# Optimization experiments

Measured on AMD Instinct MI355X. Metric: run time of the kernel, lower is better.

The kernel has to match this reference:

```python
import jax, jax.numpy as jnp
import numpy as np

N_NODES = 30000
N_REL = 8
N_EDGES = 150000
EMB = 128
HID = 128
OUT = 256
HEADS = 4
RANK = 8
SCALE = 1.0
NEG_SLOPE = 0.2
LN_EPS = 1e-5


def setup_inputs():
    key = jax.random.key(0)
    ks = jax.random.split(key, 16)
    def nrm(k, shp, s=0.05):
        return jax.random.normal(k, shp, dtype=jnp.float32) * s
    d2 = HEADS * HID  # conv2 input dim = 512
    return {
        "entity_emb": nrm(ks[0], (N_NODES, EMB)),
        "A1": nrm(ks[1], (N_REL, EMB * RANK)),
        "B1": nrm(ks[2], (N_REL, EMB * RANK)),
        "W1": nrm(ks[3], (HEADS * HID, EMB)),
        "att_l1": nrm(ks[4], (1, HEADS, HID)),
        "att_r1": nrm(ks[5], (1, HEADS, HID)),
        "relb1": jnp.zeros((N_REL, HEADS), jnp.float32),
        "bias1": jnp.zeros((HEADS * HID,), jnp.float32),
        "A2": nrm(ks[6], (N_REL, d2 * RANK)),
        "B2": nrm(ks[7], (N_REL, d2 * RANK)),
        "W2": nrm(ks[8], (OUT, d2)),
        "att_l2": nrm(ks[9], (1, 1, OUT)),
        "att_r2": nrm(ks[10], (1, 1, OUT)),
        "relb2": jnp.zeros((N_REL, 1), jnp.float32),
        "bias2": jnp.zeros((OUT,), jnp.float32),
        "res_W": nrm(ks[11], (OUT, EMB)),
        "res_b": jnp.zeros((OUT,), jnp.float32),
        "ln_g": jnp.ones((OUT,), jnp.float32),
        "ln_b": jnp.zeros((OUT,), jnp.float32),
        "edge_index": jax.random.randint(ks[12], (2, N_EDGES), 0, N_NODES),
        "edge_type": jax.random.randint(ks[13], (N_EDGES,), 0, N_REL),
    }


def _rel_gat_conv(x, A, B, W, att_l, att_r, relb, bias, j_idx, i_idx, etype, heads, out_dim, concat):
    # x: [N,d]; A,B: [R, d*k]; W: [heads*out_dim, d]
    N, d = x.shape
    R = A.shape[0]
    k = RANK
    HC = heads * out_dim
    A3 = A.reshape(R, d, k)
    B3 = B.reshape(R, d, k)
    z_all = x @ W.T  # [N, HC] base linear (shared by z_i and z_j)
    # LoRA low-rank projection per (node, relation): P[n,r] = B_r^T x_n
    P = jnp.einsum('nd,rdk->nrk', x, B3)          # [N,R,k] (small)
    low = P[j_idx, etype]                          # [E,k]
    # Fused LoRA-through-lin: lin(scale*A_r B_r^T x) = scale * low @ (A_r^T W^T)
    M = jnp.einsum('rdk,hd->rkh', A3, W).reshape(R * k, HC)  # [R*k, HC]
    oh = jax.nn.one_hot(etype, R, dtype=x.dtype)   # [E,R]
    low_exp = (oh[:, :, None] * low[:, None, :]).reshape(-1, R * k)  # [E,R*k]
    z_j = (z_all[j_idx] + SCALE * (low_exp @ M)).reshape(-1, heads, out_dim)  # [E,H,C]
    z_i = z_all[i_idx].reshape(-1, heads, out_dim)                            # [E,H,C]
    alpha = (z_i * att_l).sum(-1) + (z_j * att_r).sum(-1) + relb[etype]       # [E,H]
    alpha = jax.nn.leaky_relu(alpha, NEG_SLOPE)
    # per-relation loop => softmax groups are (relation, target node)
    seg = etype * N + i_idx
    n_seg = R * N
    amax = jax.ops.segment_max(alpha, seg, num_segments=n_seg)
    ex = jnp.exp(alpha - amax[seg])
    den = jax.ops.segment_sum(ex, seg, num_segments=n_seg)
    alpha = ex / den[seg]
    msg = z_j * alpha[:, :, None]                  # [E,H,C]
    out = jax.ops.segment_sum(msg, i_idx, num_segments=N)  # [N,H,C]
    out = out.reshape(N, HC) if concat else out.mean(axis=1)
    return out + bias


def _forward(entity_emb, A1, B1, W1, att_l1, att_r1, relb1, bias1,
             A2, B2, W2, att_l2, att_r2, relb2, bias2,
             res_W, res_b, ln_g, ln_b, edge_index, edge_type):
    j_idx, i_idx = edge_index[0], edge_index[1]
    x0 = entity_emb
    x = _rel_gat_conv(x0, A1, B1, W1, att_l1, att_r1, relb1, bias1,
                      j_idx, i_idx, edge_type, HEADS, HID, True)
    x = jax.nn.elu(x)
    x = _rel_gat_conv(x, A2, B2, W2, att_l2, att_r2, relb2, bias2,
                      j_idx, i_idx, edge_type, 1, OUT, False)
    x = x + (x0 @ res_W.T + res_b)
    mu = x.mean(axis=-1, keepdims=True)
    var = ((x - mu) ** 2).mean(axis=-1, keepdims=True)
    return (x - mu) / jnp.sqrt(var + LN_EPS) * ln_g + ln_b


def reference(entity_emb, A1, B1, W1, att_l1, att_r1, relb1, bias1,
              A2, B2, W2, att_l2, att_r2, relb2, bias2,
              res_W, res_b, ln_g, ln_b, edge_index, edge_type):
    return _forward(entity_emb, A1, B1, W1, att_l1, att_r1, relb1, bias1,
                    A2, B2, W2, att_l2, att_r2, relb2, bias2,
                    res_W, res_b, ln_g, ln_b, edge_index, edge_type)
```

## Files before the change

kernel.cpp:

```cpp
#include <hip/hip_runtime.h>
#include <cstddef>

#define NRELS 8
#define EMB 128
#define HID 128
#define OUTD 256
#define HEADS 4
#define RANK 8
#define D2 512
#define KCAT 192
#define NEG_SLOPE 0.2f
#define LN_EPS 1e-5f
#define JMASK 0x07FFFFFFu

typedef short bf16x8 __attribute__((ext_vector_type(8)));
typedef float f32x4 __attribute__((ext_vector_type(4)));

__device__ __forceinline__ unsigned short f2bf(float f) {
  union { float f; unsigned u; } v; v.f = f;
  unsigned u = v.u;
  return (unsigned short)((u + 0x7fffu + ((u >> 16) & 1u)) >> 16);
}
__device__ __forceinline__ float bf2f(unsigned short u) {
  union { unsigned u; float f; } v; v.u = (unsigned)u << 16; return v.f;
}
__device__ __forceinline__ unsigned pk2(float a, float b) {
  return (unsigned)f2bf(a) | ((unsigned)f2bf(b) << 16);
}
__device__ __forceinline__ unsigned asu(float f) { return __float_as_uint(f); }

#define GLOAD16(ldsp, gp) \
  __builtin_amdgcn_global_load_lds((const __attribute__((address_space(1))) unsigned int*)(gp), \
      (__attribute__((address_space(3))) unsigned int*)(ldsp), 16, 0, 0)

template<int BIAS, int F32OUT, int ELU, int PB>
__device__ __forceinline__ void gemm_tile_body(unsigned short* AsB, unsigned short* BsB,
    int bx, int by, int ny,
    const unsigned short* __restrict__ A, const unsigned short* __restrict__ B,
    unsigned short* __restrict__ C, float* __restrict__ Cf,
    const unsigned short* __restrict__ Bp, float* __restrict__ Cp,
    int M, int N, int K, int lda, int aoffc,
    const float* __restrict__ bias, const float* __restrict__ b1p) {
  const int tid = threadIdx.x;
  const int wave = tid >> 6;
  const int lane = tid & 63;
  const int wm = wave & 1;
  const int wn = wave >> 1;
  const int r16 = lane & 15;
  const int quad = lane >> 4;
  const int bm = bx * 128;
  const int lr = lane >> 2;
  const int lc = ((lane & 3) ^ ((lane >> 3) & 3)) * 8;
  const int rsw = (quad ^ ((r16 >> 1) & 3)) * 8;
  const bool isP = PB && (by == ny - 1);
  const unsigned short* Bu = isP ? Bp : B;
  const int bn = isP ? 0 : by * 128;
  const unsigned short* Abase = A + (size_t)by * (isP ? 0 : aoffc);
  int ar0 = bm + wave * 32 + lr;      if (ar0 >= M) ar0 = M - 1;
  int ar1 = bm + wave * 32 + 16 + lr; if (ar1 >= M) ar1 = M - 1;
  const unsigned short* Ag0 = Abase + (size_t)ar0 * lda + lc;
  const unsigned short* Ag1 = Abase + (size_t)ar1 * lda + lc;
  const unsigned short* Bg0 = Bu + (size_t)(bn + wave * 32 + lr) * K + lc;
  const unsigned short* Bg1 = Bu + (size_t)(bn + wave * 32 + 16 + lr) * K + lc;
  f32x4 acc[4][4] = {};
  GLOAD16(AsB + wave * 1024, Ag0);
  GLOAD16(AsB + wave * 1024 + 512, Ag1);
  GLOAD16(BsB + wave * 1024, Bg0);
  GLOAD16(BsB + wave * 1024 + 512, Bg1);
  __syncthreads();
  int cur = 0;
  for (int k0 = 0; k0 < K; k0 += 32) {
    if (k0 + 32 < K) {
      GLOAD16(AsB + (cur ^ 1) * 4096 + wave * 1024, Ag0 + k0 + 32);
      GLOAD16(AsB + (cur ^ 1) * 4096 + wave * 1024 + 512, Ag1 + k0 + 32);
      GLOAD16(BsB + (cur ^ 1) * 4096 + wave * 1024, Bg0 + k0 + 32);
      GLOAD16(BsB + (cur ^ 1) * 4096 + wave * 1024 + 512, Bg1 + k0 + 32);
    }
    bf16x8 af[4], bfr[4];
#pragma unroll
    for (int mi = 0; mi < 4; ++mi)
      af[mi] = *(const bf16x8*)(AsB + cur * 4096 + (wm * 64 + mi * 16 + r16) * 32 + rsw);
#pragma unroll
    for (int ni = 0; ni < 4; ++ni)
      bfr[ni] = *(const bf16x8*)(BsB + cur * 4096 + (wn * 64 + ni * 16 + r16) * 32 + rsw);
#pragma unroll
    for (int mi = 0; mi < 4; ++mi)
#pragma unroll
      for (int ni = 0; ni < 4; ++ni)
        acc[mi][ni] = __builtin_amdgcn_mfma_f32_16x16x32_bf16(af[mi], bfr[ni], acc[mi][ni], 0, 0, 0);
    __syncthreads();
    cur ^= 1;
  }
  float bcol[4];
  if (BIAS) {
#pragma unroll
    for (int ni = 0; ni < 4; ++ni) {
      int cn = bn + wn * 64 + ni * 16 + r16;
      bcol[ni] = bias[cn];
      if (F32OUT) bcol[ni] += b1p[cn];
    }
  }
#pragma unroll
  for (int mi = 0; mi < 4; ++mi)
#pragma unroll
    for (int ni = 0; ni < 4; ++ni)
#pragma unroll
      for (int r = 0; r < 4; ++r) {
        int row = bm + wm * 64 + mi * 16 + quad * 4 + r;
        if (row < M) {
          int col = wn * 64 + ni * 16 + r16;
          float v = acc[mi][ni][r];
          if (isP) {
            Cp[(size_t)row * 128 + col] = v;
          } else {
            if (BIAS) v += bcol[ni];
            if (ELU) v = v > 0.f ? v : expm1f(v);
            size_t idx = (size_t)row * N + bn + col;
            if (F32OUT) Cf[idx] = v;
            else        C[idx] = f2bf(v);
          }
        }
      }
}

template<int BIAS, int F32OUT, int ELU, int PB>
__global__ __launch_bounds__(256) void gemm_tile(const unsigned short* __restrict__ A,
    const unsigned short* __restrict__ B, unsigned short* __restrict__ C,
    float* __restrict__ Cf, const unsigned short* __restrict__ Bp,
    float* __restrict__ Cp, int M, int N, int K, int lda, int aoffc,
    const float* __restrict__ bias, const float* __restrict__ b1p) {
  __shared__ unsigned short As[2 * 4096];
  __shared__ unsigned short Bs[2 * 4096];
  gemm_tile_body<BIAS, F32OUT, ELU, PB>(As, Bs, blockIdx.x, blockIdx.y, gridDim.y,
      A, B, C, Cf, Bp, Cp, M, N, K, lda, aoffc, bias, b1p);
}

__global__ __launch_bounds__(256) void combo_abt_p1(const float* __restrict__ Amat1,
    const float* __restrict__ W1, float* __restrict__ M1o,
    const float* __restrict__ Amat2, const float* __restrict__ W2, float* __restrict__ M2o,
    const unsigned short* __restrict__ x0b, const unsigned short* __restrict__ Bp1ext,
    float* __restrict__ Cp1, int Nn) {
  __shared__ unsigned short GA[2 * 4096];
  __shared__ unsigned short GB[2 * 4096];
  const int bx = blockIdx.x;
  if (bx < 12) {
    float* As_ = (float*)GA;
    float* Bs_ = (float*)GB;
    const float* A; const float* B; float* C; int N, K, bn;
    if (bx < 8) { A = Amat1; B = W1; C = M1o; N = D2; K = EMB; bn = bx * 64; }
    else { A = Amat2; B = W2; C = M2o; N = OUTD; K = D2; bn = (bx - 8) * 64; }
    const int tid = threadIdx.x;
    const int tx = tid & 15;
    const int ty = tid >> 4;
    const int lr2 = tid & 63;
    const int lq = tid >> 6;
    float acc[4][4] = {};
    for (int k0 = 0; k0 < K; k0 += 32) {
#pragma unroll
      for (int s = 0; s < 2; ++s) {
        const int q = lq + s * 4;
        float4 va = *(const float4*)(A + (size_t)lr2 * K + k0 + q * 4);
        As_[(q * 4 + 0) * 64 + lr2] = va.x; As_[(q * 4 + 1) * 64 + lr2] = va.y;
        As_[(q * 4 + 2) * 64 + lr2] = va.z; As_[(q * 4 + 3) * 64 + lr2] = va.w;
        float4 vb = *(const float4*)(B + (size_t)(bn + lr2) * K + k0 + q * 4);
        Bs_[(q * 4 + 0) * 64 + lr2] = vb.x; Bs_[(q * 4 + 1) * 64 + lr2] = vb.y;
        Bs_[(q * 4 + 2) * 64 + lr2] = vb.z; Bs_[(q * 4 + 3) * 64 + lr2] = vb.w;
      }
      __syncthreads();
#pragma unroll
      for (int kk = 0; kk < 32; ++kk) {
        float a[4], b[4];
#pragma unroll
        for (int i2 = 0; i2 < 4; ++i2) { a[i2] = As_[kk * 64 + ty * 4 + i2]; b[i2] = Bs_[kk * 64 + tx * 4 + i2]; }
#pragma unroll
        for (int i2 = 0; i2 < 4; ++i2)
#pragma unroll
          for (int j2 = 0; j2 < 4; ++j2)
            acc[i2][j2] = fmaf(a[i2], b[j2], acc[i2][j2]);
      }
      __syncthreads();
    }
#pragma unroll
    for (int i2 = 0; i2 < 4; ++i2)
#pragma unroll
      for (int j2 = 0; j2 < 4; ++j2)
        C[(size_t)(ty * 4 + i2) * N + bn + tx * 4 + j2] = acc[i2][j2];
  } else {
    gemm_tile_body<0, 1, 0, 0>(GA, GB, bx - 12, 0, 1, x0b, Bp1ext, nullptr, Cp1,
                               nullptr, nullptr, Nn, 128, EMB, EMB, 0, nullptr, nullptr);
  }
}

__global__ void prep_all(const float* __restrict__ x0, const float* __restrict__ W1,
    const float* __restrict__ W2, const float* __restrict__ res_W,
    const float* __restrict__ A1, const float* __restrict__ A2,
    const float* __restrict__ B1, const float* __restrict__ B2,
    const float* __restrict__ attL1, const float* __restrict__ attR1,
    const float* __restrict__ attL2, const float* __restrict__ attR2,
    unsigned short* __restrict__ x0b, unsigned short* __restrict__ Acat,
    unsigned short* __restrict__ W2b, unsigned short* __restrict__ RWcat,
    float* __restrict__ Amat1, float* __restrict__ Amat2,
    unsigned short* __restrict__ Bp1ext, unsigned short* __restrict__ Bp2ext,
    unsigned short* __restrict__ Bcat1,
    float* __restrict__ awR1f, float* __restrict__ awR2f,
    const int* __restrict__ ii, int* __restrict__ ideg, int* __restrict__ prepos,
    int E, int nx0) {
  int idx = blockIdx.x * 256 + threadIdx.x;
  if (idx < E) { prepos[idx] = atomicAdd(&ideg[ii[idx]], 1); return; } idx -= E;
  if (idx < nx0) { unsigned short b = f2bf(x0[idx]); x0b[idx] = b;
    Acat[(size_t)(idx >> 7) * KCAT + (idx & 127)] = b; return; } idx -= nx0;
  if (idx < OUTD * D2) { W2b[idx] = f2bf(W2[idx]); return; } idx -= OUTD * D2;
  if (idx < OUTD * EMB) { RWcat[(size_t)(idx >> 7) * KCAT + (idx & 127)] = f2bf(res_W[idx]); return; } idx -= OUTD * EMB;
  if (idx < 64 * EMB) { int d = idx % EMB, rk = idx / EMB, k = rk & 7, r = rk >> 3;
    Amat1[idx] = A1[(size_t)r * EMB * RANK + (size_t)d * RANK + k]; return; } idx -= 64 * EMB;
  if (idx < 64 * D2) { int d = idx % D2, rk = idx / D2, k = rk & 7, r = rk >> 3;
    Amat2[idx] = A2[(size_t)r * D2 * RANK + (size_t)d * RANK + k]; return; } idx -= 64 * D2;
  if (idx < 64 * EMB) { int d = idx % EMB, rk = idx / EMB, k = rk & 7, r = rk >> 3;
    Bp1ext[idx] = f2bf(B1[(size_t)r * EMB * RANK + (size_t)d * RANK + k]); return; } idx -= 64 * EMB;
  if (idx < 64 * D2) { int d = idx % D2, rk = idx / D2, k = rk & 7, r = rk >> 3;
    Bp2ext[idx] = f2bf(B2[(size_t)r * D2 * RANK + (size_t)d * RANK + k]); return; } idx -= 64 * D2;
  if (idx < 1024) {
    int rr = idx >> 7, d = idx & 127;
    int h = rr & 3; bool isL = rr < 4;
    const float* att = isL ? attL1 : attR1;
    float s = 0.f;
    for (int c = 0; c < HID; ++c)
      s = fmaf(W1[(size_t)(h * HID + c) * EMB + d], att[h * HID + c], s);
    Bp1ext[(64 + rr) * 128 + d] = f2bf(s);
    if (!isL) awR1f[h * 128 + d] = s;
    return; } idx -= 1024;
  if (idx < 1024) {
    int rr = idx >> 9, d = idx & 511;
    const float* att = (rr == 0) ? attL2 : attR2;
    float s = 0.f;
    for (int c = 0; c < OUTD; ++c)
      s = fmaf(W2[(size_t)c * D2 + d], att[c], s);
    Bp2ext[(size_t)(64 + rr) * 512 + d] = f2bf(s);
    if (rr == 1) awR2f[d] = s;
    return; } idx -= 1024;
  if (idx < 56 * 128) { Bp1ext[72 * 128 + idx] = 0; return; } idx -= 56 * 128;
  if (idx < 62 * 512) { Bp2ext[66 * 512 + idx] = 0; return; } idx -= 62 * 512;
  if (idx < 512 * 128) { int c = idx >> 7, t = idx & 127;
    Bcat1[(size_t)c * KCAT + t] = f2bf(W1[(size_t)c * EMB + t]); }
}

__global__ __launch_bounds__(1024) void exscan_matt(const int* __restrict__ deg,
    int* __restrict__ rowstart, int n,
    const float* __restrict__ Amat1, const float* __restrict__ awR1f, float* __restrict__ Matt1,
    const float* __restrict__ Amat2, const float* __restrict__ awR2f, float* __restrict__ Matt2) {
  if (blockIdx.x == 1) {
    int t = threadIdx.x;
    if (t < 256) {
      int rk = t >> 2, h = t & 3;
      float s = 0.f;
      for (int d = 0; d < 128; ++d)
        s = fmaf(Amat1[rk * 128 + d], awR1f[h * 128 + d], s);
      Matt1[t] = s;
    }
    return;
  }
  if (blockIdx.x == 2) {
    int t = threadIdx.x;
    if (t < 64) {
      float s = 0.f;
      for (int d = 0; d < 512; ++d) s = fmaf(Amat2[t * 512 + d], awR2f[d], s);
      Matt2[t] = s;
    }
    return;
  }
  __shared__ int wsum[16];
  int t = threadIdx.x;
  int lane = t & 63, wid = t >> 6;
  int carry = 0;
  for (int base = 0; base < n; base += 8192) {
    int i0 = base + t * 8;
    int v[8];
    if (i0 + 7 < n) {
      int4 a = *(const int4*)(deg + i0);
      int4 b = *(const int4*)(deg + i0 + 4);
      v[0] = a.x; v[1] = a.y; v[2] = a.z; v[3] = a.w;
      v[4] = b.x; v[5] = b.y; v[6] = b.z; v[7] = b.w;
    } else {
#pragma unroll
      for (int q = 0; q < 8; ++q) v[q] = (i0 + q < n) ? deg[i0 + q] : 0;
    }
    int tot = 0;
#pragma unroll
    for (int q = 0; q < 8; ++q) tot += v[q];
    int x = tot;
#pragma unroll
    for (int o = 1; o < 64; o <<= 1) {
      int y = __shfl_up(x, o, 64);
      if (lane >= o) x += y;
    }
    if (lane == 63) wsum[wid] = x;
    __syncthreads();
    if (t == 0) {
      int s = carry;
      for (int w2 = 0; w2 < 16; ++w2) { int tmp = wsum[w2]; wsum[w2] = s; s += tmp; }
      carry = s;
    }
    __syncthreads();
    int ex0 = x - tot + wsum[wid];
#pragma unroll
    for (int q = 0; q < 8; ++q) {
      if (i0 + q < n) rowstart[i0 + q] = ex0;
      ex0 += v[q];
    }
    __syncthreads();
  }
  if (t == 0) rowstart[n] = carry;
}

#define FB_BLOCKS 192
__global__ void combo_fold_ea1(const float* __restrict__ M1, const float* __restrict__ M2,
    unsigned short* __restrict__ Bcat1, unsigned short* __restrict__ RWcat,
    const int* __restrict__ ji, const int* __restrict__ ii,
    const int* __restrict__ et, const int* __restrict__ rowstart,
    const int* __restrict__ prepos, const float* __restrict__ Cp1,
    const float* __restrict__ relb1, const float* __restrict__ Matt1,
    float4* __restrict__ recs1, int E) {
  const int bx = blockIdx.x;
  if (bx < FB_BLOCKS) {
    int idx = bx * 256 + threadIdx.x;
    if (idx < 512 * 64) { int c = idx >> 6, rk = idx & 63;
      Bcat1[(size_t)c * KCAT + 128 + rk] = f2bf(M1[(size_t)rk * D2 + c]); return; }
    idx -= 512 * 64;
    if (idx < 256 * 64) { int c = idx >> 6, rk = idx & 63;
      RWcat[(size_t)c * KCAT + 128 + rk] = f2bf(M2[(size_t)rk * OUTD + c]); }
    return;
  }
  int e = (bx - FB_BLOCKS) * 256 + threadIdx.x;
  if (e >= E) return;
  int j = ji[e], i = ii[e], rt = et[e];
  float4 lo0 = *(const float4*)(Cp1 + (size_t)j * 128 + rt * 8);
  float4 lo1 = *(const float4*)(Cp1 + (size_t)j * 128 + rt * 8 + 4);
  float low[RANK] = {lo0.x, lo0.y, lo0.z, lo0.w, lo1.x, lo1.y, lo1.z, lo1.w};
  float4 ali = *(const float4*)(Cp1 + (size_t)i * 128 + 64);
  float4 arj = *(const float4*)(Cp1 + (size_t)j * 128 + 68);
  float4 rb  = *(const float4*)(relb1 + rt * 4);
  float a0 = ali.x + arj.x + rb.x;
  float a1 = ali.y + arj.y + rb.y;
  float a2 = ali.z + arj.z + rb.z;
  float a3 = ali.w + arj.w + rb.w;
#pragma unroll
  for (int k = 0; k < RANK; ++k) {
    float4 mk = *(const float4*)(Matt1 + ((rt * 8 + k) << 2));
    a0 = fmaf(low[k], mk.x, a0); a1 = fmaf(low[k], mk.y, a1);
    a2 = fmaf(low[k], mk.z, a2); a3 = fmaf(low[k], mk.w, a3);
  }
  a0 = (a0 > 0.f) ? a0 : NEG_SLOPE * a0;
  a1 = (a1 > 0.f) ? a1 : NEG_SLOPE * a1;
  a2 = (a2 > 0.f) ? a2 : NEG_SLOPE * a2;
  a3 = (a3 > 0.f) ? a3 : NEG_SLOPE * a3;
  float e0 = expf(a0), e1 = expf(a1), e2 = expf(a2), e3 = expf(a3);
  unsigned pack = ((unsigned)rt << 27) | (unsigned)j;
  float4* rp = recs1 + (size_t)(rowstart[i] + prepos[e]) * 3;
  rp[0] = make_float4(__uint_as_float(pack), e0, e1, e2);
  rp[1] = make_float4(e3, __uint_as_float(pk2(low[0], low[1])),
                      __uint_as_float(pk2(low[2], low[3])),
                      __uint_as_float(pk2(low[4], low[5])));
  rp[2] = make_float4(__uint_as_float(pk2(low[6], low[7])), 0.f, 0.f, 0.f);
}

__global__ __launch_bounds__(256) void agg1f(const float4* __restrict__ recs1,
    const int* __restrict__ rowstart, const unsigned short* __restrict__ x0b,
    unsigned short* __restrict__ XQ1, int Nn) {
  __shared__ float denS[4][32];
  const int wid = threadIdx.x >> 6, lane = threadIdx.x & 63;
  const int i = blockIdx.x * 4 + wid;
  if (i >= Nn) return;
  const int rt_mine = lane >> 3, k = lane & 7;
  const int s0 = rowstart[i], deg = rowstart[i + 1] - s0;
  const float* rf = (const float*)recs1;
  const size_t xb = (size_t)i * 768;
  {
    float q0 = 0.f, q1 = 0.f, q2 = 0.f, q3 = 0.f;
    float d0 = 0.f, d1 = 0.f, d2 = 0.f, d3 = 0.f;
    float4 a0 = {}, a1 = {};
    float a2x = 0.f;
    if (deg > 0) {
      a0 = recs1[(size_t)s0 * 3]; a1 = recs1[(size_t)s0 * 3 + 1];
      a2x = rf[(size_t)s0 * 12 + 8];
    }
    const int sel = k >> 1;
    for (int p = 0; p < deg; ++p) {
      float4 b0 = a0, b1 = a1; float b2x = a2x;
      if (p + 1 < deg) {
        b0 = recs1[(size_t)(s0 + p + 1) * 3]; b1 = recs1[(size_t)(s0 + p + 1) * 3 + 1];
        b2x = rf[(size_t)(s0 + p + 1) * 12 + 8];
      }
      int rt = (int)(asu(a0.x) >> 27);
      if (rt == rt_mine) {
        float pw = (sel == 0) ? a1.y : (sel == 1) ? a1.z : (sel == 2) ? a1.w : a2x;
        unsigned pu = asu(pw);
        float lw = bf2f((unsigned short)((k & 1) ? (pu >> 16) : (pu & 0xffff)));
        q0 = fmaf(a0.y, lw, q0); q1 = fmaf(a0.z, lw, q1);
        q2 = fmaf(a0.w, lw, q2); q3 = fmaf(a1.x, lw, q3);
        d0 += a0.y; d1 += a0.z; d2 += a0.w; d3 += a1.x;
      }
      a0 = b0; a1 = b1; a2x = b2x;
    }
    float r0 = (d0 > 0.f) ? 1.f / d0 : 0.f;
    float r1 = (d1 > 0.f) ? 1.f / d1 : 0.f;
    float r2 = (d2 > 0.f) ? 1.f / d2 : 0.f;
    float r3 = (d3 > 0.f) ? 1.f / d3 : 0.f;
    XQ1[xb + 0 * 192 + 128 + lane] = f2bf(q0 * r0);
    XQ1[xb + 1 * 192 + 128 + lane] = f2bf(q1 * r1);
    XQ1[xb + 2 * 192 + 128 + lane] = f2bf(q2 * r2);
    XQ1[xb + 3 * 192 + 128 + lane] = f2bf(q3 * r3);
    if (k == 0) {
      denS[wid][rt_mine]      = r0;
      denS[wid][8 + rt_mine]  = r1;
      denS[wid][16 + rt_mine] = r2;
      denS[wid][24 + rt_mine] = r3;
    }
  }
  const int c0 = lane * 2;
  float acc[8] = {};
  float4 r0 = {}, r1 = {};
  float e30 = 0.f, e31 = 0.f;
  unsigned za = 0u;
  if (deg > 0) { r0 = recs1[(size_t)s0 * 3]; e30 = rf[(size_t)s0 * 12 + 4];
    za = *(const unsigned*)(x0b + (size_t)(asu(r0.x) & JMASK) * 128 + c0); }
  if (deg > 1) { r1 = recs1[(size_t)(s0 + 1) * 3]; e31 = rf[(size_t)(s0 + 1) * 12 + 4]; }
  for (int p = 0; p < deg; ++p) {
    float4 r2 = r1; float e32 = e31; unsigned zb = za;
    if (p + 2 < deg) { r2 = recs1[(size_t)(s0 + p + 2) * 3];
                       e32 = rf[(size_t)(s0 + p + 2) * 12 + 4]; }
    if (p + 1 < deg) zb = *(const unsigned*)(x0b + (size_t)(asu(r1.x) & JMASK) * 128 + c0);
    int rt = (int)(asu(r0.x) >> 27);
    float w0 = r0.y * denS[wid][rt];
    float w1 = r0.z * denS[wid][8 + rt];
    float w2 = r0.w * denS[wid][16 + rt];
    float w3 = e30 * denS[wid][24 + rt];
    float v0 = bf2f((unsigned short)(za & 0xffff));
    float v1 = bf2f((unsigned short)(za >> 16));
    acc[0] = fmaf(w0, v0, acc[0]); acc[1] = fmaf(w0, v1, acc[1]);
    acc[2] = fmaf(w1, v0, acc[2]); acc[3] = fmaf(w1, v1, acc[3]);
    acc[4] = fmaf(w2, v0, acc[4]); acc[5] = fmaf(w2, v1, acc[5]);
    acc[6] = fmaf(w3, v0, acc[6]); acc[7] = fmaf(w3, v1, acc[7]);
    r0 = r1; e30 = e31; r1 = r2; e31 = e32; za = zb;
  }
#pragma unroll
  for (int h = 0; h < 4; ++h) {
    unsigned pv = pk2(acc[2 * h], acc[2 * h + 1]);
    *(unsigned*)(XQ1 + xb + h * 192 + c0) = pv;
  }
}

__global__ void edge_alpha2(const int* __restrict__ ji, const int* __restrict__ ii,
                            const int* __restrict__ et, const int* __restrict__ rowstart,
                            const int* __restrict__ prepos,
                            const float* __restrict__ Cp2,
                            const float* __restrict__ relb2, const float* __restrict__ Matt2,
                            float4* __restrict__ recs2, int E) {
  int e = blockIdx.x * blockDim.x + threadIdx.x;
  if (e >= E) return;
  int j = ji[e], i = ii[e], rt = et[e];
  float4 lo0 = *(const float4*)(Cp2 + (size_t)j * 128 + rt * 8);
  float4 lo1 = *(const float4*)(Cp2 + (size_t)j * 128 + rt * 8 + 4);
  float low[RANK] = {lo0.x, lo0.y, lo0.z, lo0.w, lo1.x, lo1.y, lo1.z, lo1.w};
  float a = Cp2[(size_t)i * 128 + 64] + Cp2[(size_t)j * 128 + 65] + relb2[rt];
#pragma unroll
  for (int k = 0; k < RANK; ++k) a = fmaf(low[k], Matt2[rt * RANK + k], a);
  a = (a > 0.f) ? a : NEG_SLOPE * a;
  float ex = expf(a);
  unsigned pack = ((unsigned)rt << 27) | (unsigned)j;
  float4* rp = recs2 + (size_t)(rowstart[i] + prepos[e]) * 2;
  rp[0] = make_float4(__uint_as_float(pack), ex,
                      __uint_as_float(pk2(low[0], low[1])),
                      __uint_as_float(pk2(low[2], low[3])));
  rp[1] = make_float4(__uint_as_float(pk2(low[4], low[5])),
                      __uint_as_float(pk2(low[6], low[7])), 0.f, 0.f);
}

__global__ __launch_bounds__(256) void qden2(const float4* __restrict__ recs2,
    const int* __restrict__ rowstart, unsigned short* __restrict__ Acat,
    float* __restrict__ rden2, int Nn) {
  const int wid = threadIdx.x >> 6, lane = threadIdx.x & 63;
  const int i = blockIdx.x * 4 + wid;
  if (i >= Nn) return;
  const int rt_mine = lane >> 3, k = lane & 7;
  const int s0 = rowstart[i], deg = rowstart[i + 1] - s0;
  const float* rf = (const float*)recs2;
  float q = 0.f, d = 0.f;
  float4 a0 = {}; float2 a1 = {};
  if (deg > 0) { a0 = recs2[(size_t)s0 * 2]; a1 = *(const float2*)(rf + (size_t)s0 * 8 + 4); }
  const int sel = k >> 1;
  for (int p = 0; p < deg; ++p) {
    float4 b0 = a0; float2 b1 = a1;
    if (p + 1 < deg) {
      b0 = recs2[(size_t)(s0 + p + 1) * 2];
      b1 = *(const float2*)(rf + (size_t)(s0 + p + 1) * 8 + 4);
    }
    int rt = (int)(asu(a0.x) >> 27);
    if (rt == rt_mine) {
      float pw = (sel == 0) ? a0.z : (sel == 1) ? a0.w : (sel == 2) ? a1.x : a1.y;
      unsigned pu = asu(pw);
      float lw = bf2f((unsigned short)((k & 1) ? (pu >> 16) : (pu & 0xffff)));
      q = fmaf(a0.y, lw, q); d += a0.y;
    }
    a0 = b0; a1 = b1;
  }
  float rd = (d > 0.f) ? 1.f / d : 0.f;
  Acat[(size_t)i * KCAT + 128 + lane] = f2bf(q * rd);
  if (k == 0) rden2[(size_t)i * 8 + rt_mine] = rd;
}

__global__ __launch_bounds__(256) void node_agg2_lite(const float4* __restrict__ recs2,
    const int* __restrict__ rowstart, const unsigned short* __restrict__ z2b,
    const float* __restrict__ rden2, const float* __restrict__ o2,
    const float* __restrict__ ln_g, const float* __restrict__ ln_b,
    float* __restrict__ y, int Nn) {
  const int wid = threadIdx.x >> 6;
  const int lane = threadIdx.x & 63;
  const int i = blockIdx.x * 4 + wid;
  if (i >= Nn) return;
  __shared__ float denS[4][NRELS];
  if (lane < NRELS) denS[wid][lane] = rden2[(size_t)i * 8 + lane];
  const int s0 = rowstart[i];
  const int deg = rowstart[i + 1] - s0;
  const int c0 = lane * 4;
  float acc[4] = {};
  float4 r0 = {}, r1 = {}, r2 = {};
  uint2 za = make_uint2(0u, 0u), zb = make_uint2(0u, 0u);
  if (deg > 0) { r0 = recs2[(size_t)s0 * 2];
    za = *(const uint2*)(z2b + (size_t)(asu(r0.x) & JMASK) * OUTD + c0); }
  if (deg > 1) { r1 = recs2[(size_t)(s0 + 1) * 2];
    zb = *(const uint2*)(z2b + (size_t)(asu(r1.x) & JMASK) * OUTD + c0); }
  if (deg > 2) r2 = recs2[(size_t)(s0 + 2) * 2];
  for (int p = 0; p < deg; ++p) {
    float4 r3 = r2;
    uint2 zn = zb;
    if (p + 3 < deg) r3 = recs2[(size_t)(s0 + p + 3) * 2];
    if (p + 2 < deg)
      zn = *(const uint2*)(z2b + (size_t)(asu(r2.x) & JMASK) * OUTD + c0);
    int rt = (int)(asu(r0.x) >> 27);
    float wt = r0.y * denS[wid][rt];
    acc[0] = fmaf(wt, bf2f((unsigned short)(za.x & 0xffff)), acc[0]);
    acc[1] = fmaf(wt, bf2f((unsigned short)(za.x >> 16)), acc[1]);
    acc[2] = fmaf(wt, bf2f((unsigned short)(za.y & 0xffff)), acc[2]);
    acc[3] = fmaf(wt, bf2f((unsigned short)(za.y >> 16)), acc[3]);
    r0 = r1; r1 = r2; r2 = r3; za = zb; zb = zn;
  }
  float4 rsv = *(const float4*)(o2 + (size_t)i * OUTD + c0);
  float vv[4];
  vv[0] = acc[0] + rsv.x;
  vv[1] = acc[1] + rsv.y;
  vv[2] = acc[2] + rsv.z;
  vv[3] = acc[3] + rsv.w;
  float s = vv[0] + vv[1] + vv[2] + vv[3];
  for (int o = 32; o > 0; o >>= 1) s += __shfl_xor(s, o, 64);
  float mu = s * (1.f / OUTD);
  float q = 0.f;
#pragma unroll
  for (int k = 0; k < 4; ++k) { float d = vv[k] - mu; q += d * d; }
  for (int o = 32; o > 0; o >>= 1) q += __shfl_xor(q, o, 64);
  float rstd = rsqrtf(q * (1.f / OUTD) + LN_EPS);
  float4 g = *(const float4*)(ln_g + c0);
  float4 bb = *(const float4*)(ln_b + c0);
  float4 ov;
  ov.x = (vv[0] - mu) * rstd * g.x + bb.x;
  ov.y = (vv[1] - mu) * rstd * g.y + bb.y;
  ov.z = (vv[2] - mu) * rstd * g.z + bb.z;
  ov.w = (vv[3] - mu) * rstd * g.w + bb.w;
  *(float4*)(y + (size_t)i * OUTD + c0) = ov;
}

extern "C" void kernel_launch(void* const* d_in, const int* in_sizes, int n_in,
                              void* d_out, int out_size, void* d_ws, size_t ws_size,
                              hipStream_t stream) {
  const float* x0     = (const float*)d_in[0];
  const float* A1     = (const float*)d_in[1];
  const float* B1     = (const float*)d_in[2];
  const float* W1     = (const float*)d_in[3];
  const float* attL1  = (const float*)d_in[4];
  const float* attR1  = (const float*)d_in[5];
  const float* relb1  = (const float*)d_in[6];
  const float* bias1  = (const float*)d_in[7];
  const float* A2     = (const float*)d_in[8];
  const float* B2     = (const float*)d_in[9];
  const float* W2     = (const float*)d_in[10];
  const float* attL2  = (const float*)d_in[11];
  const float* attR2  = (const float*)d_in[12];
  const float* relb2  = (const float*)d_in[13];
  const float* bias2  = (const float*)d_in[14];
  const float* res_W  = (const float*)d_in[15];
  const float* res_b  = (const float*)d_in[16];
  const float* ln_g   = (const float*)d_in[17];
  const float* ln_b   = (const float*)d_in[18];
  const int*   eidx   = (const int*)d_in[19];
  const int*   etype  = (const int*)d_in[20];
  float* out = (float*)d_out;

  const int Nn = in_sizes[0] / EMB;
  const int E  = in_sizes[20];
  const int* ji = eidx;
  const int* ii = eidx + E;

  float* w = (float*)d_ws;
  size_t off = 0;
  float* o2    = w + off; off += (size_t)Nn * OUTD;
  float* Cp1   = w + off; off += (size_t)Nn * 128;
  float* Cp2   = w + off; off += (size_t)Nn * 128;
  float* M1    = w + off; off += 64 * D2;
  float* M2    = w + off; off += 64 * OUTD;
  float* Amat1 = w + off; off += 64 * EMB;
  float* Amat2 = w + off; off += 64 * D2;
  float* Matt1 = w + off; off += 64 * 4;
  float* Matt2 = w + off; off += 64;
  float* awR1f = w + off; off += 512;
  float* awR2f = w + off; off += 512;
  float* rden2 = w + off; off += (size_t)Nn * 8;
  float4* recs1 = (float4*)(w + off); off += (size_t)E * 12;
  float4* recs2 = (float4*)(w + off); off += (size_t)E * 8;
  unsigned short* z2b    = (unsigned short*)(w + off); off += (size_t)Nn * OUTD / 2;
  unsigned short* x0b    = (unsigned short*)(w + off); off += (size_t)Nn * EMB / 2;
  unsigned short* h1b    = (unsigned short*)(w + off); off += (size_t)Nn * D2 / 2;
  unsigned short* XQ1    = (unsigned short*)(w + off); off += (size_t)Nn * 768 / 2;
  unsigned short* W2b    = (unsigned short*)(w + off); off += (size_t)OUTD * D2 / 2;
  unsigned short* Acat   = (unsigned short*)(w + off); off += (size_t)Nn * KCAT / 2;
  unsigned short* RWcat  = (unsigned short*)(w + off); off += (size_t)OUTD * KCAT / 2;
  unsigned short* Bcat1  = (unsigned short*)(w + off); off += (size_t)512 * KCAT / 2;
  unsigned short* Bp1ext = (unsigned short*)(w + off); off += (size_t)128 * 128 / 2;
  unsigned short* Bp2ext = (unsigned short*)(w + off); off += (size_t)128 * 512 / 2;
  int* ideg     = (int*)(w + off); off += (size_t)Nn;
  int* prepos   = (int*)(w + off); off += (size_t)E;
  int* rowstart = (int*)(w + off); off += (size_t)Nn + 1;
  (void)ws_size; (void)n_in; (void)out_size;

  const int MT128 = (Nn + 127) / 128;
  const int NB4 = (Nn + 3) / 4;

  (void)hipMemsetAsync(ideg, 0, (size_t)Nn * sizeof(int), stream);
  {
    int nx0 = Nn * EMB;
    int total = E + nx0 + OUTD * D2 + OUTD * EMB + 64 * EMB + 64 * D2
              + 64 * EMB + 64 * D2 + 1024 + 1024 + 56 * 128 + 62 * 512 + 512 * 128;
    prep_all<<<(total + 255) / 256, 256, 0, stream>>>(x0, W1, W2, res_W, A1, A2, B1, B2,
        attL1, attR1, attL2, attR2, x0b, Acat, W2b, RWcat, Amat1, Amat2,
        Bp1ext, Bp2ext, Bcat1, awR1f, awR2f, ii, ideg, prepos, E, nx0);
  }

  exscan_matt<<<3, 1024, 0, stream>>>(ideg, rowstart, Nn, Amat1, awR1f, Matt1,
                                      Amat2, awR2f, Matt2);

  combo_abt_p1<<<12 + MT128, 256, 0, stream>>>(Amat1, W1, M1, Amat2, W2, M2,
                                               x0b, Bp1ext, Cp1, Nn);

  combo_fold_ea1<<<FB_BLOCKS + (E + 255) / 256, 256, 0, stream>>>(M1, M2, Bcat1, RWcat,
      ji, ii, etype, rowstart, prepos, Cp1, relb1, Matt1, recs1, E);

  agg1f<<<NB4, 256, 0, stream>>>(recs1, rowstart, x0b, XQ1, Nn);
  gemm_tile<1, 0, 1, 0><<<dim3(MT128, 4), 256, 0, stream>>>(XQ1, Bcat1, h1b, nullptr,
      nullptr, nullptr, Nn, D2, KCAT, 768, KCAT, bias1, nullptr);

  gemm_tile<0, 0, 0, 1><<<dim3(MT128, 3), 256, 0, stream>>>(h1b, W2b, z2b, nullptr,
      Bp2ext, Cp2, Nn, OUTD, D2, D2, 0, nullptr, nullptr);

  edge_alpha2<<<(E + 255) / 256, 256, 0, stream>>>(ji, ii, etype, rowstart, prepos, Cp2,
                                                   relb2, Matt2, recs2, E);
  qden2<<<NB4, 256, 0, stream>>>(recs2, rowstart, Acat, rden2, Nn);
  gemm_tile<1, 1, 0, 0><<<dim3(MT128, 2), 256, 0, stream>>>(Acat, RWcat, nullptr, o2,
      nullptr, nullptr, Nn, OUTD, KCAT, KCAT, 0, bias2, res_b);
  node_agg2_lite<<<NB4, 256, 0, stream>>>(recs2, rowstart, z2b, rden2, o2, ln_g, ln_b, out, Nn);
}
```

Baseline: 341.1 us.

## Read concatenated GEMM operand from two sources and group z2 tiles for L2 reuse

Removes the Acat concatenation buffer. The final residual GEMM now reads x0b for the first 128 K-columns and a compact Q2b buffer for the remaining 64, so prep_all and qden2 no longer write into a strided concat array. The z2 GEMM gets a dedicated kernel that remaps block IDs so each group of 8 row tiles covers all 3 column tiles together, which should improve L2 reuse of the A rows. It also hoists the residual and LN parameter loads in node_agg2_lite ahead of the edge loop to overlap their latency.

```diff
diff --git a/kernel.cpp b/kernel.cpp
--- a/kernel.cpp
+++ b/kernel.cpp
@@ -33,12 +33,13 @@
   __builtin_amdgcn_global_load_lds((const __attribute__((address_space(1))) unsigned int*)(gp), \
       (__attribute__((address_space(3))) unsigned int*)(ldsp), 16, 0, 0)
 
-template<int BIAS, int F32OUT, int ELU, int PB>
+template<int BIAS, int F32OUT, int ELU, int PB, int SPLITA>
 __device__ __forceinline__ void gemm_tile_body(unsigned short* AsB, unsigned short* BsB,
     int bx, int by, int ny,
     const unsigned short* __restrict__ A, const unsigned short* __restrict__ B,
     unsigned short* __restrict__ C, float* __restrict__ Cf,
     const unsigned short* __restrict__ Bp, float* __restrict__ Cp,
+    const unsigned short* __restrict__ A2, int lda2,
     int M, int N, int K, int lda, int aoffc,
     const float* __restrict__ bias, const float* __restrict__ b1p) {
   const int tid = threadIdx.x;
@@ -60,19 +61,27 @@
   int ar1 = bm + wave * 32 + 16 + lr; if (ar1 >= M) ar1 = M - 1;
   const unsigned short* Ag0 = Abase + (size_t)ar0 * lda + lc;
   const unsigned short* Ag1 = Abase + (size_t)ar1 * lda + lc;
+  const unsigned short* Ag0b = SPLITA ? (A2 + (size_t)ar0 * lda2 + lc) : nullptr;
+  const unsigned short* Ag1b = SPLITA ? (A2 + (size_t)ar1 * lda2 + lc) : nullptr;
   const unsigned short* Bg0 = Bu + (size_t)(bn + wave * 32 + lr) * K + lc;
   const unsigned short* Bg1 = Bu + (size_t)(bn + wave * 32 + 16 + lr) * K + lc;
+  auto srcA0 = [&](int kk) {
+    return (SPLITA && kk >= 128) ? Ag0b + (kk - 128) : Ag0 + kk;
+  };
+  auto srcA1 = [&](int kk) {
+    return (SPLITA && kk >= 128) ? Ag1b + (kk - 128) : Ag1 + kk;
+  };
   f32x4 acc[4][4] = {};
-  GLOAD16(AsB + wave * 1024, Ag0);
-  GLOAD16(AsB + wave * 1024 + 512, Ag1);
+  GLOAD16(AsB + wave * 1024, srcA0(0));
+  GLOAD16(AsB + wave * 1024 + 512, srcA1(0));
   GLOAD16(BsB + wave * 1024, Bg0);
   GLOAD16(BsB + wave * 1024 + 512, Bg1);
   __syncthreads();
   int cur = 0;
   for (int k0 = 0; k0 < K; k0 += 32) {
     if (k0 + 32 < K) {
-      GLOAD16(AsB + (cur ^ 1) * 4096 + wave * 1024, Ag0 + k0 + 32);
-      GLOAD16(AsB + (cur ^ 1) * 4096 + wave * 1024 + 512, Ag1 + k0 + 32);
+      GLOAD16(AsB + (cur ^ 1) * 4096 + wave * 1024, srcA0(k0 + 32));
+      GLOAD16(AsB + (cur ^ 1) * 4096 + wave * 1024 + 512, srcA1(k0 + 32));
       GLOAD16(BsB + (cur ^ 1) * 4096 + wave * 1024, Bg0 + k0 + 32);
       GLOAD16(BsB + (cur ^ 1) * 4096 + wave * 1024 + 512, Bg1 + k0 + 32);
     }
@@ -123,16 +132,32 @@
       }
 }
 
-template<int BIAS, int F32OUT, int ELU, int PB>
+template<int BIAS, int F32OUT, int ELU, int PB, int SPLITA>
 __global__ __launch_bounds__(256) void gemm_tile(const unsigned short* __restrict__ A,
     const unsigned short* __restrict__ B, unsigned short* __restrict__ C,
     float* __restrict__ Cf, const unsigned short* __restrict__ Bp,
-    float* __restrict__ Cp, int M, int N, int K, int lda, int aoffc,
+    float* __restrict__ Cp, const unsigned short* __restrict__ A2, int lda2,
+    int M, int N, int K, int lda, int aoffc,
     const float* __restrict__ bias, const float* __restrict__ b1p) {
   __shared__ unsigned short As[2 * 4096];
   __shared__ unsigned short Bs[2 * 4096];
-  gemm_tile_body<BIAS, F32OUT, ELU, PB>(As, Bs, blockIdx.x, blockIdx.y, gridDim.y,
-      A, B, C, Cf, Bp, Cp, M, N, K, lda, aoffc, bias, b1p);
+  gemm_tile_body<BIAS, F32OUT, ELU, PB, SPLITA>(As, Bs, blockIdx.x, blockIdx.y, gridDim.y,
+      A, B, C, Cf, Bp, Cp, A2, lda2, M, N, K, lda, aoffc, bias, b1p);
+}
+
+__global__ __launch_bounds__(256) void gemm_tile_z2(const unsigned short* __restrict__ A,
+    const unsigned short* __restrict__ B, unsigned short* __restrict__ C,
+    const unsigned short* __restrict__ Bp, float* __restrict__ Cp,
+    int M, int N, int K, int nbx) {
+  __shared__ unsigned short As[2 * 4096];
+  __shared__ unsigned short Bs[2 * 4096];
+  int id = blockIdx.x;
+  int g = id / 24, r = id % 24;
+  int by = r >> 3;
+  int bx = g * 8 + (r & 7);
+  if (bx >= nbx) return;
+  gemm_tile_body<0, 0, 0, 1, 0>(As, Bs, bx, by, 3,
+      A, B, C, nullptr, Bp, Cp, nullptr, 0, M, N, K, K, 0, nullptr, nullptr);
 }
 
 __global__ __launch_bounds__(256) void combo_abt_p1(const float* __restrict__ Amat1,
@@ -186,8 +211,8 @@
       for (int j2 = 0; j2 < 4; ++j2)
         C[(size_t)(ty * 4 + i2) * N + bn + tx * 4 + j2] = acc[i2][j2];
   } else {
-    gemm_tile_body<0, 1, 0, 0>(GA, GB, bx - 12, 0, 1, x0b, Bp1ext, nullptr, Cp1,
-                               nullptr, nullptr, Nn, 128, EMB, EMB, 0, nullptr, nullptr);
+    gemm_tile_body<0, 1, 0, 0, 0>(GA, GB, bx - 12, 0, 1, x0b, Bp1ext, nullptr, Cp1,
+        nullptr, nullptr, nullptr, 0, Nn, 128, EMB, EMB, 0, nullptr, nullptr);
   }
 }
 
@@ -197,7 +222,7 @@
     const float* __restrict__ B1, const float* __restrict__ B2,
     const float* __restrict__ attL1, const float* __restrict__ attR1,
     const float* __restrict__ attL2, const float* __restrict__ attR2,
-    unsigned short* __restrict__ x0b, unsigned short* __restrict__ Acat,
+    unsigned short* __restrict__ x0b,
     unsigned short* __restrict__ W2b, unsigned short* __restrict__ RWcat,
     float* __restrict__ Amat1, float* __restrict__ Amat2,
     unsigned short* __restrict__ Bp1ext, unsigned short* __restrict__ Bp2ext,
@@ -207,8 +232,7 @@
     int E, int nx0) {
   int idx = blockIdx.x * 256 + threadIdx.x;
   if (idx < E) { prepos[idx] = atomicAdd(&ideg[ii[idx]], 1); return; } idx -= E;
-  if (idx < nx0) { unsigned short b = f2bf(x0[idx]); x0b[idx] = b;
-    Acat[(size_t)(idx >> 7) * KCAT + (idx & 127)] = b; return; } idx -= nx0;
+  if (idx < nx0) { x0b[idx] = f2bf(x0[idx]); return; } idx -= nx0;
   if (idx < OUTD * D2) { W2b[idx] = f2bf(W2[idx]); return; } idx -= OUTD * D2;
   if (idx < OUTD * EMB) { RWcat[(size_t)(idx >> 7) * KCAT + (idx & 127)] = f2bf(res_W[idx]); return; } idx -= OUTD * EMB;
   if (idx < 64 * EMB) { int d = idx % EMB, rk = idx / EMB, k = rk & 7, r = rk >> 3;
@@ -476,7 +500,7 @@
 }
 
 __global__ __launch_bounds__(256) void qden2(const float4* __restrict__ recs2,
-    const int* __restrict__ rowstart, unsigned short* __restrict__ Acat,
+    const int* __restrict__ rowstart, unsigned short* __restrict__ Q2b,
     float* __restrict__ rden2, int Nn) {
   const int wid = threadIdx.x >> 6, lane = threadIdx.x & 63;
   const int i = blockIdx.x * 4 + wid;
@@ -504,7 +528,7 @@
     a0 = b0; a1 = b1;
   }
   float rd = (d > 0.f) ? 1.f / d : 0.f;
-  Acat[(size_t)i * KCAT + 128 + lane] = f2bf(q * rd);
+  Q2b[(size_t)i * 64 + lane] = f2bf(q * rd);
   if (k == 0) rden2[(size_t)i * 8 + rt_mine] = rd;
 }
 
@@ -522,6 +546,9 @@
   const int s0 = rowstart[i];
   const int deg = rowstart[i + 1] - s0;
   const int c0 = lane * 4;
+  float4 rsv = *(const float4*)(o2 + (size_t)i * OUTD + c0);
+  float4 g = *(const float4*)(ln_g + c0);
+  float4 bb = *(const float4*)(ln_b + c0);
   float acc[4] = {};
   float4 r0 = {}, r1 = {}, r2 = {};
   uint2 za = make_uint2(0u, 0u), zb = make_uint2(0u, 0u);
@@ -544,7 +571,6 @@
     acc[3] = fmaf(wt, bf2f((unsigned short)(za.y >> 16)), acc[3]);
     r0 = r1; r1 = r2; r2 = r3; za = zb; zb = zn;
   }
-  float4 rsv = *(const float4*)(o2 + (size_t)i * OUTD + c0);
   float vv[4];
   vv[0] = acc[0] + rsv.x;
   vv[1] = acc[1] + rsv.y;
@@ -558,8 +584,6 @@
   for (int k = 0; k < 4; ++k) { float d = vv[k] - mu; q += d * d; }
   for (int o = 32; o > 0; o >>= 1) q += __shfl_xor(q, o, 64);
   float rstd = rsqrtf(q * (1.f / OUTD) + LN_EPS);
-  float4 g = *(const float4*)(ln_g + c0);
-  float4 bb = *(const float4*)(ln_b + c0);
   float4 ov;
   ov.x = (vv[0] - mu) * rstd * g.x + bb.x;
   ov.y = (vv[1] - mu) * rstd * g.y + bb.y;
@@ -619,8 +643,8 @@
   unsigned short* x0b    = (unsigned short*)(w + off); off += (size_t)Nn * EMB / 2;
   unsigned short* h1b    = (unsigned short*)(w + off); off += (size_t)Nn * D2 / 2;
   unsigned short* XQ1    = (unsigned short*)(w + off); off += (size_t)Nn * 768 / 2;
+  unsigned short* Q2b    = (unsigned short*)(w + off); off += (size_t)Nn * 64 / 2;
   unsigned short* W2b    = (unsigned short*)(w + off); off += (size_t)OUTD * D2 / 2;
-  unsigned short* Acat   = (unsigned short*)(w + off); off += (size_t)Nn * KCAT / 2;
   unsigned short* RWcat  = (unsigned short*)(w + off); off += (size_t)OUTD * KCAT / 2;
   unsigned short* Bcat1  = (unsigned short*)(w + off); off += (size_t)512 * KCAT / 2;
   unsigned short* Bp1ext = (unsigned short*)(w + off); off += (size_t)128 * 128 / 2;
@@ -639,7 +663,7 @@
     int total = E + nx0 + OUTD * D2 + OUTD * EMB + 64 * EMB + 64 * D2
               + 64 * EMB + 64 * D2 + 1024 + 1024 + 56 * 128 + 62 * 512 + 512 * 128;
     prep_all<<<(total + 255) / 256, 256, 0, stream>>>(x0, W1, W2, res_W, A1, A2, B1, B2,
-        attL1, attR1, attL2, attR2, x0b, Acat, W2b, RWcat, Amat1, Amat2,
+        attL1, attR1, attL2, attR2, x0b, W2b, RWcat, Amat1, Amat2,
         Bp1ext, Bp2ext, Bcat1, awR1f, awR2f, ii, ideg, prepos, E, nx0);
   }
 
@@ -653,16 +677,19 @@
       ji, ii, etype, rowstart, prepos, Cp1, relb1, Matt1, recs1, E);
 
   agg1f<<<NB4, 256, 0, stream>>>(recs1, rowstart, x0b, XQ1, Nn);
-  gemm_tile<1, 0, 1, 0><<<dim3(MT128, 4), 256, 0, stream>>>(XQ1, Bcat1, h1b, nullptr,
-      nullptr, nullptr, Nn, D2, KCAT, 768, KCAT, bias1, nullptr);
-
-  gemm_tile<0, 0, 0, 1><<<dim3(MT128, 3), 256, 0, stream>>>(h1b, W2b, z2b, nullptr,
-      Bp2ext, Cp2, Nn, OUTD, D2, D2, 0, nullptr, nullptr);
+  gemm_tile<1, 0, 1, 0, 0><<<dim3(MT128, 4), 256, 0, stream>>>(XQ1, Bcat1, h1b, nullptr,
+      nullptr, nullptr, nullptr, 0, Nn, D2, KCAT, 768, KCAT, bias1, nullptr);
+
+  {
+    int ngrp = (MT128 + 7) / 8;
+    gemm_tile_z2<<<ngrp * 24, 256, 0, stream>>>(h1b, W2b, z2b, Bp2ext, Cp2,
+                                                Nn, OUTD, D2, MT128);
+  }
 
   edge_alpha2<<<(E + 255) / 256, 256, 0, stream>>>(ji, ii, etype, rowstart, prepos, Cp2,
                                                    relb2, Matt2, recs2, E);
-  qden2<<<NB4, 256, 0, stream>>>(recs2, rowstart, Acat, rden2, Nn);
-  gemm_tile<1, 1, 0, 0><<<dim3(MT128, 2), 256, 0, stream>>>(Acat, RWcat, nullptr, o2,
-      nullptr, nullptr, Nn, OUTD, KCAT, KCAT, 0, bias2, res_b);
+  qden2<<<NB4, 256, 0, stream>>>(recs2, rowstart, Q2b, rden2, Nn);
+  gemm_tile<1, 1, 0, 0, 1><<<dim3(MT128, 2), 256, 0, stream>>>(x0b, RWcat, nullptr, o2,
+      nullptr, nullptr, Q2b, 64, Nn, OUTD, KCAT, EMB, 0, bias2, res_b);
   node_agg2_lite<<<NB4, 256, 0, stream>>>(recs2, rowstart, z2b, rden2, o2, ln_g, ln_b, out, Nn);
 }
```

New measurement: 337.4 us. Within noise of the previous version (-1.1%).
